# Optimization experiments

Measured on AMD Instinct MI355X. Metric: run time of the kernel, lower is better.

The kernel has to match this reference:

```python
import jax, jax.numpy as jnp
import numpy as np

# Static problem constants (must match setup_inputs)
NUM_GRAPHS = 64      # batch_size = int(batch[-1]) + 1
PTS_PER_GRAPH = 512
RATIO = 16           # centroids per graph
HEADS = 4
IN_CH = 64           # = out_channels per head (concat=False -> mean over heads)
NEG_SLOPE = 0.2


def setup_inputs() -> dict:
    key = jax.random.key(0)
    ks = jax.random.split(key, 8)
    N = NUM_GRAPHS * PTS_PER_GRAPH
    x = jax.random.normal(ks[0], (N, IN_CH), dtype=jnp.float32)
    edge_index = jnp.zeros((2, 2), dtype=jnp.int64)  # unused by forward
    batch = (jnp.arange(N) // PTS_PER_GRAPH).astype(jnp.int64)
    xcent_base = jax.random.normal(ks[1], (RATIO, IN_CH), dtype=jnp.float32)
    W_l = jax.random.normal(ks[2], (IN_CH, HEADS * IN_CH), dtype=jnp.float32) / np.sqrt(IN_CH)
    b_l = jax.random.normal(ks[3], (HEADS * IN_CH,), dtype=jnp.float32) * 0.01
    W_r = jax.random.normal(ks[4], (IN_CH, HEADS * IN_CH), dtype=jnp.float32) / np.sqrt(IN_CH)
    b_r = jax.random.normal(ks[5], (HEADS * IN_CH,), dtype=jnp.float32) * 0.01
    att = jax.random.normal(ks[6], (HEADS, IN_CH), dtype=jnp.float32) / np.sqrt(IN_CH)
    bias = jax.random.normal(ks[7], (IN_CH,), dtype=jnp.float32) * 0.01
    return {"x": x, "edge_index": edge_index, "batch": batch,
            "xcent_base": xcent_base, "W_l": W_l, "b_l": b_l,
            "W_r": W_r, "b_r": b_r, "att": att, "bias": bias}


def _bipart_pool(x, batch, xcent_base, W_l, b_l, W_r, b_r, att, bias):
    N = x.shape[0]
    B = NUM_GRAPHS
    Nc = B * RATIO  # number of centroid (target) nodes

    # Dense bipartite edges: each source node -> all RATIO centroids of its graph.
    src = jnp.repeat(jnp.arange(N, dtype=jnp.int32), RATIO)                     # [E]
    dst = jnp.tile(jnp.arange(RATIO, dtype=jnp.int32), N) \
        + jnp.repeat(batch.astype(jnp.int32), RATIO) * RATIO                    # [E]

    # PyG GATv2Conv(add_self_loops=True): remove src==dst edges, then add
    # self loops (i,i) for i < min(N_src, N_dst) = Nc. Keep static shapes by
    # masking the removed edges instead of deleting them.
    self_idx = jnp.arange(Nc, dtype=jnp.int32)
    src_f = jnp.concatenate([src, self_idx])
    dst_f = jnp.concatenate([dst, self_idx])
    drop = jnp.concatenate([src == dst, jnp.zeros((Nc,), dtype=bool)])          # [E+Nc]

    # Linear projections (source and target sides)
    x_l = (x @ W_l + b_l).reshape(N, HEADS, IN_CH)                              # [N,H,C]
    xcent = jnp.tile(xcent_base, (B, 1))                                        # [Nc,IN]
    x_r = (xcent @ W_r + b_r).reshape(Nc, HEADS, IN_CH)                         # [Nc,H,C]

    # GATv2 attention: leaky_relu(x_i + x_j) . att, softmax per target node
    xj = x_l[src_f]                                                             # [E',H,C]
    g = jax.nn.leaky_relu(xj + x_r[dst_f], NEG_SLOPE)
    alpha = jnp.einsum('ehc,hc->eh', g, att)                                    # [E',H]
    alpha = jnp.where(drop[:, None], jnp.float32(-1e30), alpha)
    amax = jax.ops.segment_max(alpha, dst_f, num_segments=Nc)                   # [Nc,H]
    e = jnp.exp(alpha - amax[dst_f])
    den = jax.ops.segment_sum(e, dst_f, num_segments=Nc)                        # [Nc,H]
    w = e / den[dst_f]                                                          # [E',H]

    out = jax.ops.segment_sum(w[..., None] * xj, dst_f, num_segments=Nc)        # [Nc,H,C]
    out = out.mean(axis=1) + bias                                               # concat=False -> mean heads
    return out.reshape(B, RATIO, IN_CH)


def reference(x, edge_index, batch, xcent_base, W_l, b_l, W_r, b_r, att, bias):
    xcent = _bipart_pool(x, batch, xcent_base, W_l, b_l, W_r, b_r, att, bias)
    batchcent = jnp.repeat(jnp.arange(NUM_GRAPHS, dtype=jnp.int64), RATIO)
    return xcent, batchcent
```

## Files before the change

kernel.cpp:

```cpp
#include <hip/hip_runtime.h>

#define PTS 512
#define CH  64
#define NC  1024

using s8v = __attribute__((ext_vector_type(8))) short;
using f4v = __attribute__((ext_vector_type(4))) float;

static __device__ __forceinline__ unsigned short f2b(float f) {
    unsigned u = __float_as_uint(f);
    return (unsigned short)((u + 0x7FFFu + ((u >> 16) & 1u)) >> 16);
}
static __device__ __forceinline__ float b2f(unsigned short s) {
    return __uint_as_float((unsigned)s << 16);
}

__global__ __launch_bounds__(256) void k0(
    const float* __restrict__ xcb, const float* __restrict__ W_r,
    const float* __restrict__ b_r, const float* __restrict__ att,
    const float* __restrict__ W_l,
    float* __restrict__ xr_ws, float* __restrict__ sxr_ws,
    unsigned short* __restrict__ Wt)
{
    __shared__ float s_row[256];
    const int blk = blockIdx.x, tid = threadIdx.x;
    if (blk < 16) {
        const int h = blk >> 2, rq = blk & 3;
        const int rl = tid >> 6, c = tid & 63;
        const int r = rq * 4 + rl;
        float acc = b_r[h * 64 + c];
        for (int k = 0; k < 64; ++k)
            acc = fmaf(xcb[r * 64 + k], W_r[k * 256 + h * 64 + c], acc);
        xr_ws[(h * 16 + r) * 64 + c] = acc;
        s_row[rl * 64 + c] = acc;
        __syncthreads();
        if (tid < 4) {
            float s = 0.f;
            for (int cc = 0; cc < 64; ++cc)
                s = fmaf(s_row[tid * 64 + cc], att[h * 64 + cc], s);
            sxr_ws[h * 16 + rq * 4 + tid] = s;
        }
    } else {
        int base = (blk - 16) * 2048;
        for (int t = tid; t < 2048; t += 256) {
            int idx = base + t;
            int h = idx >> 12, ch = (idx >> 6) & 63, k = idx & 63;
            Wt[idx] = f2b(W_l[k * 256 + h * 64 + ch]);
        }
    }
}

__global__ __launch_bounds__(256, 2) void k1(
    const float* __restrict__ x, const unsigned short* __restrict__ Wt,
    const float* __restrict__ b_l, const float* __restrict__ att,
    const float* __restrict__ xr_ws, const float* __restrict__ sxr_ws,
    const float* __restrict__ bias,
    float* __restrict__ aws, unsigned short* __restrict__ xlself,
    float* __restrict__ out)
{
    __shared__ unsigned short s_xl[64 * 264];

    const int tid = threadIdx.x;
    const int lane = tid & 63;
    const int w = __builtin_amdgcn_readfirstlane(tid >> 6);
    const int blk = blockIdx.x;
    const int row0 = blk * 64;
    const int l15 = lane & 15, quad = lane >> 4;

    f4v acc[4][4];
    const f4v zf = {0.f, 0.f, 0.f, 0.f};
#pragma unroll
    for (int m = 0; m < 4; ++m)
#pragma unroll
        for (int n = 0; n < 4; ++n) acc[m][n] = zf;

#pragma unroll
    for (int ks = 0; ks < 2; ++ks) {
        s8v Af[4], Bf[4];
#pragma unroll
        for (int m = 0; m < 4; ++m) {
            const float* xp = x + (size_t)(row0 + m * 16 + l15) * 64 + ks * 32 + quad * 8;
            float4 u0 = *(const float4*)xp;
            float4 u1 = *(const float4*)(xp + 4);
            s8v a;
            a[0] = (short)f2b(u0.x); a[1] = (short)f2b(u0.y);
            a[2] = (short)f2b(u0.z); a[3] = (short)f2b(u0.w);
            a[4] = (short)f2b(u1.x); a[5] = (short)f2b(u1.y);
            a[6] = (short)f2b(u1.z); a[7] = (short)f2b(u1.w);
            Af[m] = a;
        }
#pragma unroll
        for (int n = 0; n < 4; ++n)
            Bf[n] = *(const s8v*)(Wt + (size_t)(w * 64 + n * 16 + l15) * 64
                                  + ks * 32 + quad * 8);
#pragma unroll
        for (int m = 0; m < 4; ++m)
#pragma unroll
            for (int n = 0; n < 4; ++n)
                acc[m][n] = __builtin_amdgcn_mfma_f32_16x16x32_bf16(
                    Af[m], Bf[n], acc[m][n], 0, 0, 0);
    }

    float blv[4];
#pragma unroll
    for (int n = 0; n < 4; ++n) blv[n] = b_l[w * 64 + n * 16 + l15];
#pragma unroll
    for (int m = 0; m < 4; ++m)
#pragma unroll
        for (int n = 0; n < 4; ++n) {
            int ch = w * 64 + n * 16 + l15;
#pragma unroll
            for (int qq = 0; qq < 4; ++qq) {
                int row = m * 16 + quad * 4 + qq;
                s_xl[row * 264 + ch] = f2b(acc[m][n][qq] + blv[n]);
            }
        }

    if (blk >= 16 && blk < 20) {
        int base = (blk - 16) * 16384;
        float bv = bias[tid & 63];
#pragma unroll
        for (int j = 0; j < 64; ++j) out[base + j * 256 + tid] = bv;
    }
    if (blk == 20) {
#pragma unroll
        for (int j = 0; j < 4; ++j) {
            int c = j * 256 + tid;
            out[65536 + c] = (float)(c >> 4);
        }
    }

    __syncthreads();

    if (blk < 16) {
#pragma unroll
        for (int t = 0; t < 8; ++t) {
            int idx = tid + t * 256;
            int row = idx >> 5, co = (idx & 31) * 8;
            uint4 v = *(const uint4*)&s_xl[row * 264 + co];
            *(uint4*)&xlself[(size_t)(row0 + row) * 256 + co] = v;
        }
    }

    const float* attw = att + w * 64;
    const float* xrw  = xr_ws + w * 1024;
    float ac[16];
#pragma unroll
    for (int r = 0; r < 16; ++r) ac[r] = 0.f;
    float sxl = 0.f;

#pragma unroll
    for (int half = 0; half < 2; ++half) {
        const int cb = half * 32;
        float xlv[32], atv[32];
#pragma unroll
        for (int c8 = 0; c8 < 4; ++c8) {
            uint4 raw = *(const uint4*)&s_xl[lane * 264 + w * 64 + cb + c8 * 8];
            unsigned uu[4] = {raw.x, raw.y, raw.z, raw.w};
#pragma unroll
            for (int p = 0; p < 4; ++p) {
                xlv[c8 * 8 + 2 * p]     = __uint_as_float(uu[p] << 16);
                xlv[c8 * 8 + 2 * p + 1] = __uint_as_float(uu[p] & 0xffff0000u);
            }
        }
#pragma unroll
        for (int cq = 0; cq < 8; ++cq) {
            float4 a4 = *(const float4*)(attw + cb + cq * 4);
            atv[cq * 4 + 0] = a4.x; atv[cq * 4 + 1] = a4.y;
            atv[cq * 4 + 2] = a4.z; atv[cq * 4 + 3] = a4.w;
        }
#pragma unroll
        for (int t = 0; t < 32; ++t) sxl = fmaf(atv[t], xlv[t], sxl);

#pragma unroll 2
        for (int r = 0; r < 16; ++r) {
            const float4* xrp = (const float4*)(xrw + r * 64 + cb);
            float a = 0.f;
#pragma unroll
            for (int cq = 0; cq < 8; ++cq) {
                float4 x4 = xrp[cq];
                a = fmaf(atv[cq * 4 + 0], fabsf(xlv[cq * 4 + 0] + x4.x), a);
                a = fmaf(atv[cq * 4 + 1], fabsf(xlv[cq * 4 + 1] + x4.y), a);
                a = fmaf(atv[cq * 4 + 2], fabsf(xlv[cq * 4 + 2] + x4.z), a);
                a = fmaf(atv[cq * 4 + 3], fabsf(xlv[cq * 4 + 3] + x4.w), a);
            }
            ac[r] += a;
        }
    }

    float* ap = aws + ((size_t)(blk >> 3) * 4 + w) * 8192 + (blk & 7) * 64 + lane;
#pragma unroll
    for (int r = 0; r < 16; ++r)
        ap[r * 512] = 0.6f * (sxl + sxr_ws[w * 16 + r]) + 0.4f * ac[r];
}

__global__ __launch_bounds__(512, 1) void k2(
    const float* __restrict__ x, const float* __restrict__ W_l,
    const float* __restrict__ b_l, const float* __restrict__ aws,
    const unsigned short* __restrict__ xlself, float* __restrict__ out)
{
    __shared__ float s_et[8192];
    __shared__ float sW[4096];
    __shared__ float s_y[1024];
    __shared__ float s_m[16], s_inv[16], s_f[16];

    const int bh = blockIdx.x, b = bh >> 2, h = bh & 3;
    const int tid = threadIdx.x;
    const float* abh = aws + (size_t)bh * 8192;

    for (int idx = tid; idx < 4096; idx += 512)
        sW[idx] = W_l[(idx >> 6) * 256 + h * 64 + (idx & 63)];
    for (int idx = tid; idx < 8192; idx += 512) {
        int r = idx >> 9, i = idx & 511;
        s_et[i * 16 + r] = abh[idx];
    }

    {
        const int r = tid >> 5, lg = tid & 31;
        const int snode = b * 16 + r;
        const float a_self = aws[(size_t)((snode >> 9) * 4 + h) * 8192
                                 + r * 512 + (snode & 511)];
        float m = a_self;
        for (int j = 0; j < 16; ++j) {
            int i = lg + j * 32;
            float a = abh[r * 512 + i];
            if (b == 0 && i == r) a = -1e30f;
            m = fmaxf(m, a);
        }
#pragma unroll
        for (int off = 16; off >= 1; off >>= 1) m = fmaxf(m, __shfl_xor(m, off));
        float d = 0.f;
        for (int j = 0; j < 16; ++j) {
            int i = lg + j * 32;
            float a = abh[r * 512 + i];
            d += (b == 0 && i == r) ? 0.f : __expf(a - m);
        }
#pragma unroll
        for (int off = 16; off >= 1; off >>= 1) d += __shfl_xor(d, off);
        if (lg == 0) {
            float es = __expf(a_self - m);
            float inv = 1.f / (d + es);
            s_m[r] = m; s_inv[r] = inv; s_f[r] = es * inv;
        }
    }
    __syncthreads();

    for (int idx = tid; idx < 8192; idx += 512) {
        int i = idx >> 4, r = idx & 15;
        float a = s_et[idx];
        float e = (b == 0 && i == r) ? 0.f : __expf(a - s_m[r]) * s_inv[r];
        s_et[idx] = e;
    }
    __syncthreads();

    const int kt = tid & 15, rt = (tid >> 4) & 3, is = tid >> 6;
    float y4[4][4];
#pragma unroll
    for (int i = 0; i < 4; ++i)
#pragma unroll
        for (int j = 0; j < 4; ++j) y4[i][j] = 0.f;

    const float* xb = x + ((size_t)b * PTS + is * 64) * 64;
#pragma unroll 4
    for (int ii = 0; ii < 64; ++ii) {
        float4 xv = *(const float4*)(xb + ii * 64 + kt * 4);
        float4 ev = *(const float4*)&s_et[(is * 64 + ii) * 16 + rt * 4];
        y4[0][0] = fmaf(ev.x, xv.x, y4[0][0]); y4[0][1] = fmaf(ev.x, xv.y, y4[0][1]);
        y4[0][2] = fmaf(ev.x, xv.z, y4[0][2]); y4[0][3] = fmaf(ev.x, xv.w, y4[0][3]);
        y4[1][0] = fmaf(ev.y, xv.x, y4[1][0]); y4[1][1] = fmaf(ev.y, xv.y, y4[1][1]);
        y4[1][2] = fmaf(ev.y, xv.z, y4[1][2]); y4[1][3] = fmaf(ev.y, xv.w, y4[1][3]);
        y4[2][0] = fmaf(ev.z, xv.x, y4[2][0]); y4[2][1] = fmaf(ev.z, xv.y, y4[2][1]);
        y4[2][2] = fmaf(ev.z, xv.z, y4[2][2]); y4[2][3] = fmaf(ev.z, xv.w, y4[2][3]);
        y4[3][0] = fmaf(ev.w, xv.x, y4[3][0]); y4[3][1] = fmaf(ev.w, xv.y, y4[3][1]);
        y4[3][2] = fmaf(ev.w, xv.z, y4[3][2]); y4[3][3] = fmaf(ev.w, xv.w, y4[3][3]);
    }
    __syncthreads();

#pragma unroll
    for (int rr = 0; rr < 4; ++rr)
        *(float4*)&s_et[is * 1024 + (rt * 4 + rr) * 64 + kt * 4] =
            make_float4(y4[rr][0], y4[rr][1], y4[rr][2], y4[rr][3]);
    __syncthreads();

    for (int o = tid; o < 1024; o += 512) {
        float s = 0.f;
#pragma unroll
        for (int sl = 0; sl < 8; ++sl) s += s_et[sl * 1024 + o];
        s_y[o] = s;
    }
    __syncthreads();

    for (int o = tid; o < 1024; o += 512) {
        int r = o >> 6, ch = o & 63;
        float a = 0.f;
#pragma unroll
        for (int k = 0; k < 64; ++k)
            a = fmaf(s_y[r * 64 + k], sW[k * 64 + ch], a);
        float f = s_f[r];
        float val = a + (1.f - f) * b_l[h * 64 + ch]
                  + f * b2f(xlself[(size_t)(b * 16 + r) * 256 + h * 64 + ch]);
        atomicAdd(&out[(b * 16 + r) * 64 + ch], 0.25f * val);
    }
}

extern "C" void kernel_launch(void* const* d_in, const int* in_sizes, int n_in,
                              void* d_out, int out_size, void* d_ws, size_t ws_size,
                              hipStream_t stream) {
    (void)in_sizes; (void)n_in; (void)out_size; (void)ws_size;
    const float* x    = (const float*)d_in[0];
    const float* xcb  = (const float*)d_in[3];
    const float* W_l  = (const float*)d_in[4];
    const float* b_l  = (const float*)d_in[5];
    const float* W_r  = (const float*)d_in[6];
    const float* b_r  = (const float*)d_in[7];
    const float* att  = (const float*)d_in[8];
    const float* bias = (const float*)d_in[9];
    float* out = (float*)d_out;

    float* wsf = (float*)d_ws;
    float*          aws    = wsf;
    float*          xr_ws  = wsf + 2097152;
    float*          sxr_ws = wsf + 2101248;
    unsigned short* Wt     = (unsigned short*)(wsf + 2101376);
    unsigned short* xlself = (unsigned short*)(wsf + 2109568);

    hipLaunchKernelGGL(k0, dim3(24), dim3(256), 0, stream,
                       xcb, W_r, b_r, att, W_l, xr_ws, sxr_ws, Wt);
    hipLaunchKernelGGL(k1, dim3(512), dim3(256), 0, stream,
                       x, Wt, b_l, att, xr_ws, sxr_ws, bias, aws, xlself, out);
    hipLaunchKernelGGL(k2, dim3(256), dim3(512), 0, stream,
                       x, W_l, b_l, aws, xlself, out);
}
```

Baseline: 118.9 us.

## Fuse score computation and softmax-aggregation kernels into one per-graph-head kernel

Merges the attention-score kernel and the aggregation kernel into a single kernel that handles one graph and one head per block. The x_l tile and the per-target scores stay in swizzled shared memory instead of making a round trip through an 8 MB global workspace. The bias/batch output initialisation and the fp32 self-loop x_l rows move into the small first kernel, and the bf16 W transpose is now done per block into LDS. The cost is heavier LDS use per block and occupancy of one 512-thread block per CU, with W_l converted redundantly in every block.

```diff
diff --git a/kernel.cpp b/kernel.cpp
--- a/kernel.cpp
+++ b/kernel.cpp
@@ -2,7 +2,6 @@
 
 #define PTS 512
 #define CH  64
-#define NC  1024
 
 using s8v = __attribute__((ext_vector_type(8))) short;
 using f4v = __attribute__((ext_vector_type(4))) float;
@@ -11,16 +10,14 @@
     unsigned u = __float_as_uint(f);
     return (unsigned short)((u + 0x7FFFu + ((u >> 16) & 1u)) >> 16);
 }
-static __device__ __forceinline__ float b2f(unsigned short s) {
-    return __uint_as_float((unsigned)s << 16);
-}
 
 __global__ __launch_bounds__(256) void k0(
     const float* __restrict__ xcb, const float* __restrict__ W_r,
     const float* __restrict__ b_r, const float* __restrict__ att,
-    const float* __restrict__ W_l,
+    const float* __restrict__ x,   const float* __restrict__ W_l,
+    const float* __restrict__ b_l, const float* __restrict__ bias,
     float* __restrict__ xr_ws, float* __restrict__ sxr_ws,
-    unsigned short* __restrict__ Wt)
+    float* __restrict__ xlself_ws, float* __restrict__ out)
 {
     __shared__ float s_row[256];
     const int blk = blockIdx.x, tid = threadIdx.x;
@@ -40,190 +37,212 @@
                 s = fmaf(s_row[tid * 64 + cc], att[h * 64 + cc], s);
             sxr_ws[h * 16 + rq * 4 + tid] = s;
         }
+    } else if (blk < 80) {
+        const int g0 = (blk - 16) * 16;
+        float acc[16];
+        const float blv = b_l[tid];
+#pragma unroll
+        for (int j = 0; j < 16; ++j) acc[j] = blv;
+        for (int k = 0; k < 64; ++k) {
+            const float wv = W_l[k * 256 + tid];
+#pragma unroll
+            for (int j = 0; j < 16; ++j)
+                acc[j] = fmaf(x[(size_t)(g0 + j) * 64 + k], wv, acc[j]);
+        }
+#pragma unroll
+        for (int j = 0; j < 16; ++j)
+            xlself_ws[(size_t)(g0 + j) * 256 + tid] = acc[j];
+    } else if (blk < 144) {
+        const int base = (blk - 80) * 1024 + tid * 4;
+        float4 bv = *(const float4*)(bias + ((tid * 4) & 63));
+        *(float4*)(out + base) = bv;
     } else {
-        int base = (blk - 16) * 2048;
-        for (int t = tid; t < 2048; t += 256) {
-            int idx = base + t;
-            int h = idx >> 12, ch = (idx >> 6) & 63, k = idx & 63;
-            Wt[idx] = f2b(W_l[k * 256 + h * 64 + ch]);
-        }
+        const int c = tid * 4;
+        *(float4*)(out + 65536 + c) = make_float4(
+            (float)(c >> 4), (float)((c + 1) >> 4),
+            (float)((c + 2) >> 4), (float)((c + 3) >> 4));
     }
 }
 
-__global__ __launch_bounds__(256, 2) void k1(
-    const float* __restrict__ x, const unsigned short* __restrict__ Wt,
+__global__ __launch_bounds__(512, 1) void kmain(
+    const float* __restrict__ x, const float* __restrict__ W_l,
     const float* __restrict__ b_l, const float* __restrict__ att,
     const float* __restrict__ xr_ws, const float* __restrict__ sxr_ws,
-    const float* __restrict__ bias,
-    float* __restrict__ aws, unsigned short* __restrict__ xlself,
-    float* __restrict__ out)
+    const float* __restrict__ xlself_ws, float* __restrict__ out)
 {
-    __shared__ unsigned short s_xl[64 * 264];
+    __shared__ __align__(16) float s_buf[16384];
+    __shared__ __align__(16) float s_alpha[8192];
+    __shared__ __align__(16) unsigned short s_wt[4096];
+    __shared__ float s_W[4096];
+    __shared__ float s_aself[16], s_m[16], s_inv[16], s_f[16];
+
+    unsigned short* s_xl  = (unsigned short*)s_buf;
+    float*          s_part = s_buf;
+    float*          s_y    = s_buf + 8192;
 
     const int tid = threadIdx.x;
-    const int lane = tid & 63;
-    const int w = __builtin_amdgcn_readfirstlane(tid >> 6);
-    const int blk = blockIdx.x;
-    const int row0 = blk * 64;
-    const int l15 = lane & 15, quad = lane >> 4;
-
-    f4v acc[4][4];
-    const f4v zf = {0.f, 0.f, 0.f, 0.f};
-#pragma unroll
-    for (int m = 0; m < 4; ++m)
-#pragma unroll
-        for (int n = 0; n < 4; ++n) acc[m][n] = zf;
-
-#pragma unroll
-    for (int ks = 0; ks < 2; ++ks) {
-        s8v Af[4], Bf[4];
-#pragma unroll
-        for (int m = 0; m < 4; ++m) {
-            const float* xp = x + (size_t)(row0 + m * 16 + l15) * 64 + ks * 32 + quad * 8;
-            float4 u0 = *(const float4*)xp;
-            float4 u1 = *(const float4*)(xp + 4);
-            s8v a;
-            a[0] = (short)f2b(u0.x); a[1] = (short)f2b(u0.y);
-            a[2] = (short)f2b(u0.z); a[3] = (short)f2b(u0.w);
-            a[4] = (short)f2b(u1.x); a[5] = (short)f2b(u1.y);
-            a[6] = (short)f2b(u1.z); a[7] = (short)f2b(u1.w);
-            Af[m] = a;
-        }
-#pragma unroll
-        for (int n = 0; n < 4; ++n)
-            Bf[n] = *(const s8v*)(Wt + (size_t)(w * 64 + n * 16 + l15) * 64
-                                  + ks * 32 + quad * 8);
+    const int h = blockIdx.x >> 6;
+    const int b = blockIdx.x & 63;
+
+    {
+        const int c = tid >> 3, kk0 = (tid & 7) * 8;
+        s8v wv;
+#pragma unroll
+        for (int j = 0; j < 8; ++j)
+            wv[j] = (short)f2b(W_l[(kk0 + j) * 256 + h * 64 + c]);
+        *(s8v*)&s_wt[c * 64 + (kk0 ^ ((c & 7) << 3))] = wv;
+
+        for (int idx = tid; idx < 4096; idx += 512)
+            s_W[idx] = W_l[(idx >> 6) * 256 + h * 64 + (idx & 63)];
+
+        const int r = tid >> 5, lg = tid & 31;
+        float sxs = 0.f, ab = 0.f;
+#pragma unroll
+        for (int j = 0; j < 2; ++j) {
+            const int cc = lg * 2 + j;
+            const float at  = att[h * 64 + cc];
+            const float xrv = xr_ws[(h * 16 + r) * 64 + cc];
+            const float xsv = xlself_ws[(size_t)(b * 16 + r) * 256 + h * 64 + cc];
+            sxs = fmaf(at, xsv, sxs);
+            ab  = fmaf(at, fabsf(xsv + xrv), ab);
+        }
+#pragma unroll
+        for (int off = 16; off >= 1; off >>= 1) {
+            sxs += __shfl_xor(sxs, off);
+            ab  += __shfl_xor(ab, off);
+        }
+        if (lg == 0)
+            s_aself[r] = 0.6f * (sxs + sxr_ws[h * 16 + r]) + 0.4f * ab;
+    }
+    __syncthreads();
+
+    {
+        const int lane = tid & 63, w = tid >> 6;
+        const int l15 = lane & 15, quad = lane >> 4;
+        const size_t row0 = (size_t)b * PTS + w * 64;
+        f4v acc[4][4];
+        const f4v zf = {0.f, 0.f, 0.f, 0.f};
 #pragma unroll
         for (int m = 0; m < 4; ++m)
 #pragma unroll
-            for (int n = 0; n < 4; ++n)
-                acc[m][n] = __builtin_amdgcn_mfma_f32_16x16x32_bf16(
-                    Af[m], Bf[n], acc[m][n], 0, 0, 0);
-    }
-
-    float blv[4];
-#pragma unroll
-    for (int n = 0; n < 4; ++n) blv[n] = b_l[w * 64 + n * 16 + l15];
-#pragma unroll
-    for (int m = 0; m < 4; ++m)
-#pragma unroll
-        for (int n = 0; n < 4; ++n) {
-            int ch = w * 64 + n * 16 + l15;
-#pragma unroll
-            for (int qq = 0; qq < 4; ++qq) {
-                int row = m * 16 + quad * 4 + qq;
-                s_xl[row * 264 + ch] = f2b(acc[m][n][qq] + blv[n]);
-            }
-        }
-
-    if (blk >= 16 && blk < 20) {
-        int base = (blk - 16) * 16384;
-        float bv = bias[tid & 63];
-#pragma unroll
-        for (int j = 0; j < 64; ++j) out[base + j * 256 + tid] = bv;
-    }
-    if (blk == 20) {
-#pragma unroll
-        for (int j = 0; j < 4; ++j) {
-            int c = j * 256 + tid;
-            out[65536 + c] = (float)(c >> 4);
-        }
-    }
-
-    __syncthreads();
-
-    if (blk < 16) {
-#pragma unroll
-        for (int t = 0; t < 8; ++t) {
-            int idx = tid + t * 256;
-            int row = idx >> 5, co = (idx & 31) * 8;
-            uint4 v = *(const uint4*)&s_xl[row * 264 + co];
-            *(uint4*)&xlself[(size_t)(row0 + row) * 256 + co] = v;
-        }
-    }
-
-    const float* attw = att + w * 64;
-    const float* xrw  = xr_ws + w * 1024;
-    float ac[16];
-#pragma unroll
-    for (int r = 0; r < 16; ++r) ac[r] = 0.f;
-    float sxl = 0.f;
-
-#pragma unroll
-    for (int half = 0; half < 2; ++half) {
-        const int cb = half * 32;
-        float xlv[32], atv[32];
-#pragma unroll
-        for (int c8 = 0; c8 < 4; ++c8) {
-            uint4 raw = *(const uint4*)&s_xl[lane * 264 + w * 64 + cb + c8 * 8];
-            unsigned uu[4] = {raw.x, raw.y, raw.z, raw.w};
-#pragma unroll
-            for (int p = 0; p < 4; ++p) {
-                xlv[c8 * 8 + 2 * p]     = __uint_as_float(uu[p] << 16);
-                xlv[c8 * 8 + 2 * p + 1] = __uint_as_float(uu[p] & 0xffff0000u);
-            }
-        }
-#pragma unroll
-        for (int cq = 0; cq < 8; ++cq) {
-            float4 a4 = *(const float4*)(attw + cb + cq * 4);
-            atv[cq * 4 + 0] = a4.x; atv[cq * 4 + 1] = a4.y;
-            atv[cq * 4 + 2] = a4.z; atv[cq * 4 + 3] = a4.w;
-        }
-#pragma unroll
-        for (int t = 0; t < 32; ++t) sxl = fmaf(atv[t], xlv[t], sxl);
+            for (int n = 0; n < 4; ++n) acc[m][n] = zf;
+
+#pragma unroll
+        for (int ks = 0; ks < 2; ++ks) {
+            s8v Af[4], Bf[4];
+#pragma unroll
+            for (int m = 0; m < 4; ++m) {
+                const float* xp = x + (row0 + m * 16 + l15) * 64 + ks * 32 + quad * 8;
+                float4 u0 = *(const float4*)xp;
+                float4 u1 = *(const float4*)(xp + 4);
+                s8v a;
+                a[0] = (short)f2b(u0.x); a[1] = (short)f2b(u0.y);
+                a[2] = (short)f2b(u0.z); a[3] = (short)f2b(u0.w);
+                a[4] = (short)f2b(u1.x); a[5] = (short)f2b(u1.y);
+                a[6] = (short)f2b(u1.z); a[7] = (short)f2b(u1.w);
+                Af[m] = a;
+            }
+#pragma unroll
+            for (int n = 0; n < 4; ++n) {
+                const int cc = n * 16 + l15;
+                Bf[n] = *(const s8v*)&s_wt[cc * 64 +
+                        ((ks * 32 + quad * 8) ^ ((cc & 7) << 3))];
+            }
+#pragma unroll
+            for (int m = 0; m < 4; ++m)
+#pragma unroll
+                for (int n = 0; n < 4; ++n)
+                    acc[m][n] = __builtin_amdgcn_mfma_f32_16x16x32_bf16(
+                        Af[m], Bf[n], acc[m][n], 0, 0, 0);
+        }
+
+        float blv[4];
+#pragma unroll
+        for (int n = 0; n < 4; ++n) blv[n] = b_l[h * 64 + n * 16 + l15];
+#pragma unroll
+        for (int m = 0; m < 4; ++m)
+#pragma unroll
+            for (int n = 0; n < 4; ++n) {
+                const int cc = n * 16 + l15;
+#pragma unroll
+                for (int qq = 0; qq < 4; ++qq) {
+                    const int row = w * 64 + m * 16 + quad * 4 + qq;
+                    s_xl[row * 64 + (cc ^ ((row & 7) << 3))] =
+                        f2b(acc[m][n][qq] + blv[n]);
+                }
+            }
+    }
+    __syncthreads();
+
+    {
+        const int i = tid, sw = i & 3, xsw = (i & 7) << 3;
+        const float* attw = att + h * 64;
+        const float* xrw  = xr_ws + h * 1024;
+        float ac[16];
+#pragma unroll
+        for (int r = 0; r < 16; ++r) ac[r] = 0.f;
+        float sxl = 0.f;
+
+#pragma unroll
+        for (int half = 0; half < 2; ++half) {
+            const int cb = half * 32;
+            float xlv[32], atv[32];
+#pragma unroll
+            for (int c8 = 0; c8 < 4; ++c8) {
+                const int ch0 = cb + c8 * 8;
+                uint4 raw = *(const uint4*)&s_xl[i * 64 + (ch0 ^ xsw)];
+                unsigned uu[4] = {raw.x, raw.y, raw.z, raw.w};
+#pragma unroll
+                for (int p = 0; p < 4; ++p) {
+                    xlv[c8 * 8 + 2 * p]     = __uint_as_float(uu[p] << 16);
+                    xlv[c8 * 8 + 2 * p + 1] = __uint_as_float(uu[p] & 0xffff0000u);
+                }
+            }
+#pragma unroll
+            for (int cq = 0; cq < 8; ++cq) {
+                float4 a4 = *(const float4*)(attw + cb + cq * 4);
+                atv[cq * 4 + 0] = a4.x; atv[cq * 4 + 1] = a4.y;
+                atv[cq * 4 + 2] = a4.z; atv[cq * 4 + 3] = a4.w;
+            }
+#pragma unroll
+            for (int t = 0; t < 32; ++t) sxl = fmaf(atv[t], xlv[t], sxl);
 
 #pragma unroll 2
-        for (int r = 0; r < 16; ++r) {
-            const float4* xrp = (const float4*)(xrw + r * 64 + cb);
-            float a = 0.f;
-#pragma unroll
-            for (int cq = 0; cq < 8; ++cq) {
-                float4 x4 = xrp[cq];
-                a = fmaf(atv[cq * 4 + 0], fabsf(xlv[cq * 4 + 0] + x4.x), a);
-                a = fmaf(atv[cq * 4 + 1], fabsf(xlv[cq * 4 + 1] + x4.y), a);
-                a = fmaf(atv[cq * 4 + 2], fabsf(xlv[cq * 4 + 2] + x4.z), a);
-                a = fmaf(atv[cq * 4 + 3], fabsf(xlv[cq * 4 + 3] + x4.w), a);
-            }
-            ac[r] += a;
-        }
-    }
-
-    float* ap = aws + ((size_t)(blk >> 3) * 4 + w) * 8192 + (blk & 7) * 64 + lane;
-#pragma unroll
-    for (int r = 0; r < 16; ++r)
-        ap[r * 512] = 0.6f * (sxl + sxr_ws[w * 16 + r]) + 0.4f * ac[r];
-}
-
-__global__ __launch_bounds__(512, 1) void k2(
-    const float* __restrict__ x, const float* __restrict__ W_l,
-    const float* __restrict__ b_l, const float* __restrict__ aws,
-    const unsigned short* __restrict__ xlself, float* __restrict__ out)
-{
-    __shared__ float s_et[8192];
-    __shared__ float sW[4096];
-    __shared__ float s_y[1024];
-    __shared__ float s_m[16], s_inv[16], s_f[16];
-
-    const int bh = blockIdx.x, b = bh >> 2, h = bh & 3;
-    const int tid = threadIdx.x;
-    const float* abh = aws + (size_t)bh * 8192;
-
-    for (int idx = tid; idx < 4096; idx += 512)
-        sW[idx] = W_l[(idx >> 6) * 256 + h * 64 + (idx & 63)];
-    for (int idx = tid; idx < 8192; idx += 512) {
-        int r = idx >> 9, i = idx & 511;
-        s_et[i * 16 + r] = abh[idx];
-    }
+            for (int r = 0; r < 16; ++r) {
+                const float4* xrp = (const float4*)(xrw + r * 64 + cb);
+                float a = 0.f;
+#pragma unroll
+                for (int cq = 0; cq < 8; ++cq) {
+                    float4 x4 = xrp[cq];
+                    a = fmaf(atv[cq * 4 + 0], fabsf(xlv[cq * 4 + 0] + x4.x), a);
+                    a = fmaf(atv[cq * 4 + 1], fabsf(xlv[cq * 4 + 1] + x4.y), a);
+                    a = fmaf(atv[cq * 4 + 2], fabsf(xlv[cq * 4 + 2] + x4.z), a);
+                    a = fmaf(atv[cq * 4 + 3], fabsf(xlv[cq * 4 + 3] + x4.w), a);
+                }
+                ac[r] += a;
+            }
+        }
+        float av[16];
+#pragma unroll
+        for (int r = 0; r < 16; ++r)
+            av[r] = 0.6f * (sxl + sxr_ws[h * 16 + r]) + 0.4f * ac[r];
+        float4* sa4 = (float4*)s_alpha;
+#pragma unroll
+        for (int q = 0; q < 4; ++q) {
+            float4 v = make_float4(av[q * 4 + 0], av[q * 4 + 1],
+                                   av[q * 4 + 2], av[q * 4 + 3]);
+            sa4[i * 4 + (q ^ sw)] = v;
+        }
+    }
+    __syncthreads();
 
     {
         const int r = tid >> 5, lg = tid & 31;
-        const int snode = b * 16 + r;
-        const float a_self = aws[(size_t)((snode >> 9) * 4 + h) * 8192
-                                 + r * 512 + (snode & 511)];
+        const float a_self = s_aself[r];
         float m = a_self;
         for (int j = 0; j < 16; ++j) {
-            int i = lg + j * 32;
-            float a = abh[r * 512 + i];
+            const int i = lg + j * 32;
+            float a = s_alpha[(i << 4) + (r ^ ((i & 3) << 2))];
             if (b == 0 && i == r) a = -1e30f;
             m = fmaxf(m, a);
         }
@@ -231,74 +250,85 @@
         for (int off = 16; off >= 1; off >>= 1) m = fmaxf(m, __shfl_xor(m, off));
         float d = 0.f;
         for (int j = 0; j < 16; ++j) {
-            int i = lg + j * 32;
-            float a = abh[r * 512 + i];
+            const int i = lg + j * 32;
+            float a = s_alpha[(i << 4) + (r ^ ((i & 3) << 2))];
             d += (b == 0 && i == r) ? 0.f : __expf(a - m);
         }
 #pragma unroll
         for (int off = 16; off >= 1; off >>= 1) d += __shfl_xor(d, off);
         if (lg == 0) {
-            float es = __expf(a_self - m);
-            float inv = 1.f / (d + es);
+            const float es = __expf(a_self - m);
+            const float inv = 1.f / (d + es);
             s_m[r] = m; s_inv[r] = inv; s_f[r] = es * inv;
         }
     }
     __syncthreads();
 
-    for (int idx = tid; idx < 8192; idx += 512) {
-        int i = idx >> 4, r = idx & 15;
-        float a = s_et[idx];
-        float e = (b == 0 && i == r) ? 0.f : __expf(a - s_m[r]) * s_inv[r];
-        s_et[idx] = e;
-    }
-    __syncthreads();
-
-    const int kt = tid & 15, rt = (tid >> 4) & 3, is = tid >> 6;
-    float y4[4][4];
-#pragma unroll
-    for (int i = 0; i < 4; ++i)
-#pragma unroll
-        for (int j = 0; j < 4; ++j) y4[i][j] = 0.f;
-
-    const float* xb = x + ((size_t)b * PTS + is * 64) * 64;
+    {
+        const int i = tid, sw = i & 3;
+        float4* sa4 = (float4*)s_alpha;
+#pragma unroll
+        for (int p = 0; p < 4; ++p) {
+            float4 v = sa4[i * 4 + p];
+            const int r0 = (p ^ sw) * 4;
+            v.x = (b == 0 && i == r0 + 0) ? 0.f : __expf(v.x - s_m[r0 + 0]) * s_inv[r0 + 0];
+            v.y = (b == 0 && i == r0 + 1) ? 0.f : __expf(v.y - s_m[r0 + 1]) * s_inv[r0 + 1];
+            v.z = (b == 0 && i == r0 + 2) ? 0.f : __expf(v.z - s_m[r0 + 2]) * s_inv[r0 + 2];
+            v.w = (b == 0 && i == r0 + 3) ? 0.f : __expf(v.w - s_m[r0 + 3]) * s_inv[r0 + 3];
+            sa4[i * 4 + p] = v;
+        }
+    }
+    __syncthreads();
+
+    {
+        const int kt = tid & 15, rt = (tid >> 4) & 3, is = tid >> 6;
+        float y4[4][4];
+#pragma unroll
+        for (int i = 0; i < 4; ++i)
+#pragma unroll
+            for (int j = 0; j < 4; ++j) y4[i][j] = 0.f;
+
+        const float* xb = x + ((size_t)b * PTS + is * 64) * 64;
+        const float4* sa4 = (const float4*)s_alpha;
 #pragma unroll 4
-    for (int ii = 0; ii < 64; ++ii) {
-        float4 xv = *(const float4*)(xb + ii * 64 + kt * 4);
-        float4 ev = *(const float4*)&s_et[(is * 64 + ii) * 16 + rt * 4];
-        y4[0][0] = fmaf(ev.x, xv.x, y4[0][0]); y4[0][1] = fmaf(ev.x, xv.y, y4[0][1]);
-        y4[0][2] = fmaf(ev.x, xv.z, y4[0][2]); y4[0][3] = fmaf(ev.x, xv.w, y4[0][3]);
-        y4[1][0] = fmaf(ev.y, xv.x, y4[1][0]); y4[1][1] = fmaf(ev.y, xv.y, y4[1][1]);
-        y4[1][2] = fmaf(ev.y, xv.z, y4[1][2]); y4[1][3] = fmaf(ev.y, xv.w, y4[1][3]);
-        y4[2][0] = fmaf(ev.z, xv.x, y4[2][0]); y4[2][1] = fmaf(ev.z, xv.y, y4[2][1]);
-        y4[2][2] = fmaf(ev.z, xv.z, y4[2][2]); y4[2][3] = fmaf(ev.z, xv.w, y4[2][3]);
-        y4[3][0] = fmaf(ev.w, xv.x, y4[3][0]); y4[3][1] = fmaf(ev.w, xv.y, y4[3][1]);
-        y4[3][2] = fmaf(ev.w, xv.z, y4[3][2]); y4[3][3] = fmaf(ev.w, xv.w, y4[3][3]);
-    }
-    __syncthreads();
-
-#pragma unroll
-    for (int rr = 0; rr < 4; ++rr)
-        *(float4*)&s_et[is * 1024 + (rt * 4 + rr) * 64 + kt * 4] =
-            make_float4(y4[rr][0], y4[rr][1], y4[rr][2], y4[rr][3]);
+        for (int ii = 0; ii < 64; ++ii) {
+            float4 xv = *(const float4*)(xb + ii * 64 + kt * 4);
+            const int i = is * 64 + ii;
+            float4 ev = sa4[i * 4 + (rt ^ (i & 3))];
+            y4[0][0] = fmaf(ev.x, xv.x, y4[0][0]); y4[0][1] = fmaf(ev.x, xv.y, y4[0][1]);
+            y4[0][2] = fmaf(ev.x, xv.z, y4[0][2]); y4[0][3] = fmaf(ev.x, xv.w, y4[0][3]);
+            y4[1][0] = fmaf(ev.y, xv.x, y4[1][0]); y4[1][1] = fmaf(ev.y, xv.y, y4[1][1]);
+            y4[1][2] = fmaf(ev.y, xv.z, y4[1][2]); y4[1][3] = fmaf(ev.y, xv.w, y4[1][3]);
+            y4[2][0] = fmaf(ev.z, xv.x, y4[2][0]); y4[2][1] = fmaf(ev.z, xv.y, y4[2][1]);
+            y4[2][2] = fmaf(ev.z, xv.z, y4[2][2]); y4[2][3] = fmaf(ev.z, xv.w, y4[2][3]);
+            y4[3][0] = fmaf(ev.w, xv.x, y4[3][0]); y4[3][1] = fmaf(ev.w, xv.y, y4[3][1]);
+            y4[3][2] = fmaf(ev.w, xv.z, y4[3][2]); y4[3][3] = fmaf(ev.w, xv.w, y4[3][3]);
+        }
+#pragma unroll
+        for (int rr = 0; rr < 4; ++rr)
+            *(float4*)&s_part[is * 1024 + (rt * 4 + rr) * 64 + kt * 4] =
+                make_float4(y4[rr][0], y4[rr][1], y4[rr][2], y4[rr][3]);
+    }
     __syncthreads();
 
     for (int o = tid; o < 1024; o += 512) {
         float s = 0.f;
 #pragma unroll
-        for (int sl = 0; sl < 8; ++sl) s += s_et[sl * 1024 + o];
+        for (int sl = 0; sl < 8; ++sl) s += s_part[sl * 1024 + o];
         s_y[o] = s;
     }
     __syncthreads();
 
     for (int o = tid; o < 1024; o += 512) {
-        int r = o >> 6, ch = o & 63;
+        const int r = o >> 6, ch = o & 63;
         float a = 0.f;
+        const float* yr = s_y + r * 64;
 #pragma unroll
         for (int k = 0; k < 64; ++k)
-            a = fmaf(s_y[r * 64 + k], sW[k * 64 + ch], a);
-        float f = s_f[r];
+            a = fmaf(yr[k], s_W[k * 64 + ch], a);
+        const float f = s_f[r];
         float val = a + (1.f - f) * b_l[h * 64 + ch]
-                  + f * b2f(xlself[(size_t)(b * 16 + r) * 256 + h * 64 + ch]);
+                  + f * xlself_ws[(size_t)(b * 16 + r) * 256 + h * 64 + ch];
         atomicAdd(&out[(b * 16 + r) * 64 + ch], 0.25f * val);
     }
 }
@@ -318,16 +348,13 @@
     float* out = (float*)d_out;
 
     float* wsf = (float*)d_ws;
-    float*          aws    = wsf;
-    float*          xr_ws  = wsf + 2097152;
-    float*          sxr_ws = wsf + 2101248;
-    unsigned short* Wt     = (unsigned short*)(wsf + 2101376);
-    unsigned short* xlself = (unsigned short*)(wsf + 2109568);
-
-    hipLaunchKernelGGL(k0, dim3(24), dim3(256), 0, stream,
-                       xcb, W_r, b_r, att, W_l, xr_ws, sxr_ws, Wt);
-    hipLaunchKernelGGL(k1, dim3(512), dim3(256), 0, stream,
-                       x, Wt, b_l, att, xr_ws, sxr_ws, bias, aws, xlself, out);
-    hipLaunchKernelGGL(k2, dim3(256), dim3(512), 0, stream,
-                       x, W_l, b_l, aws, xlself, out);
+    float* xr_ws     = wsf;
+    float* sxr_ws    = wsf + 4096;
+    float* xlself_ws = wsf + 4224;
+
+    hipLaunchKernelGGL(k0, dim3(145), dim3(256), 0, stream,
+                       xcb, W_r, b_r, att, x, W_l, b_l, bias,
+                       xr_ws, sxr_ws, xlself_ws, out);
+    hipLaunchKernelGGL(kmain, dim3(256), dim3(512), 0, stream,
+                       x, W_l, b_l, att, xr_ws, sxr_ws, xlself_ws, out);
 }
```

Measured after the change: 118.2 us. Within noise of the previous version (-0.6%).
